# Kernel tuning notes

Hardware: AMD Instinct MI355X
Metric: run time of the kernel (lower is better)

Reference implementation:

```python
import jax, jax.numpy as jnp
import numpy as np

Z = 64
P = Z * Z
H = 4  # hDim_1 = hDim_2 = 2*iDim with iDim=2
EPS = 1e-5
WVAR = 0.1  # WEIGHT_VARIANCE stand-in


def setup_inputs() -> dict:
    key = jax.random.key(0)
    ks = jax.random.split(key, 8)
    B = 4096
    x = jax.random.normal(ks[0], (B, Z), dtype=jnp.float32)
    W1 = jax.random.normal(ks[1], (P, 2, H), dtype=jnp.float32) * WVAR
    b1 = jax.random.normal(ks[2], (P, H), dtype=jnp.float32) * WVAR
    g1 = jnp.ones((P, H), dtype=jnp.float32)
    be1 = jnp.zeros((P, H), dtype=jnp.float32)
    W2 = jax.random.normal(ks[3], (P, H, H), dtype=jnp.float32) * WVAR
    b2 = jax.random.normal(ks[4], (P, H), dtype=jnp.float32) * WVAR
    g2 = jnp.ones((P, H), dtype=jnp.float32)
    be2 = jnp.zeros((P, H), dtype=jnp.float32)
    W3 = jax.random.normal(ks[5], (P, H), dtype=jnp.float32) * WVAR
    b3 = jax.random.normal(ks[6], (P,), dtype=jnp.float32) * WVAR
    return {"x": x, "W1": W1, "b1": b1, "g1": g1, "be1": be1,
            "W2": W2, "b2": b2, "g2": g2, "be2": be2,
            "W3": W3, "b3": b3, "dtPt": B}


def _layernorm(h, g, b):
    # LayerNorm over last dim (size H), biased variance, eps=1e-5 (torch default)
    m = jnp.mean(h, axis=-1, keepdims=True)
    v = jnp.mean(jnp.square(h - m), axis=-1, keepdims=True)
    return (h - m) * jax.lax.rsqrt(v + EPS) * g + b


def reference(x, W1, b1, g1, be1, W2, b2, g2, be2, W3, b3, dtPt):
    B = x.shape[0]
    # pairs[b, z*Z+zp] = (x[b,z], x[b,zp])  -> [B, P, 2]
    a = jnp.broadcast_to(x[:, :, None], (B, Z, Z)).reshape(B, P)
    c = jnp.broadcast_to(x[:, None, :], (B, Z, Z)).reshape(B, P)
    pair = jnp.stack([a, c], axis=-1)  # [B, P, 2]
    h = jnp.einsum('bpi,pih->bph', pair, W1) + b1
    h = _layernorm(jnp.tanh(h), g1, be1)
    h = jnp.einsum('bph,phk->bpk', h, W2) + b2
    h = _layernorm(jnp.tanh(h), g2, be2)
    out = jnp.einsum('bph,ph->bp', h, W3) + b3
    out = jax.nn.sigmoid(out)
    return out.reshape(B, Z, Z)
```

## Files before the change

kernel.cpp:

```cpp
#include <hip/hip_runtime.h>
#include <cstddef>

#define ZDIM 64
#define PDIM 4096
#define PB   256
#define BCHUNK 32

__device__ __forceinline__ float fast_tanh(float x) {
    float e = __builtin_amdgcn_exp2f(x * 2.8853900817779268f);
    float r = __builtin_amdgcn_rcpf(e + 1.0f);
    return __builtin_fmaf(-2.0f, r, 1.0f);
}

__device__ __forceinline__ float fast_sigmoid(float x) {
    float e = __builtin_amdgcn_exp2f(x * -1.4426950408889634f);
    return __builtin_amdgcn_rcpf(e + 1.0f);
}

__global__ void __launch_bounds__(PB) pair_mlp_kernel(
    const float* __restrict__ x,
    const float* __restrict__ W1, const float* __restrict__ b1,
    const float* __restrict__ g1, const float* __restrict__ be1,
    const float* __restrict__ W2, const float* __restrict__ b2,
    const float* __restrict__ g2, const float* __restrict__ be2,
    const float* __restrict__ W3, const float* __restrict__ b3,
    float* __restrict__ out, int nbc)
{
    const int tid = threadIdx.x;
    const int pb  = blockIdx.x / nbc;
    const int bc  = blockIdx.x - pb * nbc;
    const int p   = pb * PB + tid;
    const int z   = __builtin_amdgcn_readfirstlane(p >> 6);
    const int zp  = p & 63;

    const float4* W1v = reinterpret_cast<const float4*>(W1 + (size_t)p * 8);
    const float4 w1x = W1v[0];
    const float4 w1y = W1v[1];
    const float4 b1v  = reinterpret_cast<const float4*>(b1)[p];
    const float4 g1v  = reinterpret_cast<const float4*>(g1)[p];
    const float4 be1v = reinterpret_cast<const float4*>(be1)[p];

    float w2[4][4];
    {
        const float4* W2v = reinterpret_cast<const float4*>(W2 + (size_t)p * 16);
        #pragma unroll
        for (int i = 0; i < 4; ++i) {
            float4 r = W2v[i];
            w2[i][0] = r.x; w2[i][1] = r.y; w2[i][2] = r.z; w2[i][3] = r.w;
        }
    }
    const float4 b2v  = reinterpret_cast<const float4*>(b2)[p];
    const float4 g2v  = reinterpret_cast<const float4*>(g2)[p];
    const float4 be2v = reinterpret_cast<const float4*>(be2)[p];
    const float4 w3v  = reinterpret_cast<const float4*>(W3)[p];
    const float  b3s  = b3[p];

    const float w1aa[4] = {w1x.x, w1x.y, w1x.z, w1x.w};
    const float w1ba[4] = {w1y.x, w1y.y, w1y.z, w1y.w};
    const float b1a[4]  = {b1v.x, b1v.y, b1v.z, b1v.w};
    const float g1a[4]  = {g1v.x, g1v.y, g1v.z, g1v.w};
    const float be1a[4] = {be1v.x, be1v.y, be1v.z, be1v.w};
    const float b2a[4]  = {b2v.x, b2v.y, b2v.z, b2v.w};
    const float g2a[4]  = {g2v.x, g2v.y, g2v.z, g2v.w};
    const float be2a[4] = {be2v.x, be2v.y, be2v.z, be2v.w};
    const float w3a[4]  = {w3v.x, w3v.y, w3v.z, w3v.w};

    float w2g[4][4], cs2[4], b2p[4];
    #pragma unroll
    for (int j = 0; j < 4; ++j) { cs2[j] = 0.f; b2p[j] = b2a[j]; }
    #pragma unroll
    for (int i = 0; i < 4; ++i) {
        #pragma unroll
        for (int j = 0; j < 4; ++j) {
            float wg = g1a[i] * w2[i][j];
            w2g[i][j] = wg;
            cs2[j] += wg;
            b2p[j] = __builtin_fmaf(be1a[i], w2[i][j], b2p[j]);
        }
    }
    float w3g[4], cs3 = 0.f, b3p = b3s;
    #pragma unroll
    for (int j = 0; j < 4; ++j) {
        w3g[j] = g2a[j] * w3a[j];
        cs3 += w3g[j];
        b3p = __builtin_fmaf(be2a[j], w3a[j], b3p);
    }

    const int b0 = bc * BCHUNK;
    for (int it = 0; it < BCHUNK; ++it) {
        const int b = b0 + it;
        const float a = x[b * ZDIM + z];
        const float c = x[b * ZDIM + zp];

        float t[4];
        #pragma unroll
        for (int i = 0; i < 4; ++i)
            t[i] = fast_tanh(__builtin_fmaf(a, w1aa[i],
                         __builtin_fmaf(c, w1ba[i], b1a[i])));

        float s1 = (t[0] + t[1]) + (t[2] + t[3]);
        float s2 = __builtin_fmaf(t[0], t[0],
                   __builtin_fmaf(t[1], t[1],
                   __builtin_fmaf(t[2], t[2], t[3] * t[3])));
        float m  = 0.25f * s1;
        float v  = __builtin_fmaf(0.25f, s2, -(m * m));
        float rs = __builtin_amdgcn_rsqf(v + 1e-5f);

        float u[4];
        #pragma unroll
        for (int j = 0; j < 4; ++j) {
            float acc = -m * cs2[j];
            #pragma unroll
            for (int i = 0; i < 4; ++i)
                acc = __builtin_fmaf(t[i], w2g[i][j], acc);
            u[j] = fast_tanh(__builtin_fmaf(rs, acc, b2p[j]));
        }

        float q1 = (u[0] + u[1]) + (u[2] + u[3]);
        float q2 = __builtin_fmaf(u[0], u[0],
                   __builtin_fmaf(u[1], u[1],
                   __builtin_fmaf(u[2], u[2], u[3] * u[3])));
        float m2  = 0.25f * q1;
        float v2  = __builtin_fmaf(0.25f, q2, -(m2 * m2));
        float rs2 = __builtin_amdgcn_rsqf(v2 + 1e-5f);

        float acc = -m2 * cs3;
        #pragma unroll
        for (int j = 0; j < 4; ++j)
            acc = __builtin_fmaf(u[j], w3g[j], acc);

        out[(size_t)b * PDIM + p] = fast_sigmoid(__builtin_fmaf(rs2, acc, b3p));
    }
}

extern "C" void kernel_launch(void* const* d_in, const int* in_sizes, int n_in,
                              void* d_out, int out_size, void* d_ws, size_t ws_size,
                              hipStream_t stream) {
    const float* x   = (const float*)d_in[0];
    const float* W1  = (const float*)d_in[1];
    const float* b1  = (const float*)d_in[2];
    const float* g1  = (const float*)d_in[3];
    const float* be1 = (const float*)d_in[4];
    const float* W2  = (const float*)d_in[5];
    const float* b2  = (const float*)d_in[6];
    const float* g2  = (const float*)d_in[7];
    const float* be2 = (const float*)d_in[8];
    const float* W3  = (const float*)d_in[9];
    const float* b3  = (const float*)d_in[10];
    float* out = (float*)d_out;

    const int B   = in_sizes[0] / ZDIM;
    const int nbc = B / BCHUNK;
    const int grid = (PDIM / PB) * nbc;

    hipLaunchKernelGGL(pair_mlp_kernel, dim3(grid), dim3(PB), 0, stream,
                       x, W1, b1, g1, be1, W2, b2, g2, be2, W3, b3, out, nbc);
}
```

Measured before the change: 148.5 us.

## Pack batch pairs into v2f FMA and replace exp-based tanh with rational approx

Processes four batch rows per loop iteration, held in two-wide float vectors, so the arithmetic can map onto packed FP32 FMA instructions. Replaces the exp2+rcp tanh with a Padé-style rational polynomial that needs only one reciprocal and otherwise uses packed FMAs, moving work off the transcendental unit. Also adds a minimum-occupancy hint to launch bounds. The rational approximation loses accuracy for large inputs because it does not saturate at ±1, and the wider unroll raises register pressure.

```diff
diff --git a/kernel.cpp b/kernel.cpp
--- a/kernel.cpp
+++ b/kernel.cpp
@@ -6,10 +6,25 @@
 #define PB   256
 #define BCHUNK 32
 
-__device__ __forceinline__ float fast_tanh(float x) {
-    float e = __builtin_amdgcn_exp2f(x * 2.8853900817779268f);
-    float r = __builtin_amdgcn_rcpf(e + 1.0f);
-    return __builtin_fmaf(-2.0f, r, 1.0f);
+typedef float v2f __attribute__((ext_vector_type(2)));
+
+__device__ __forceinline__ v2f pkfma(v2f a, v2f b, v2f c) {
+    return __builtin_elementwise_fma(a, b, c);
+}
+
+__device__ __forceinline__ v2f splat(float s) { v2f r; r.x = s; r.y = s; return r; }
+
+__device__ __forceinline__ v2f tanh2(v2f x) {
+    v2f t = x * x;
+    v2f np = t + splat(378.0f);
+    np = pkfma(np, t, splat(17325.0f));
+    np = pkfma(np, t, splat(135135.0f));
+    v2f dp = pkfma(splat(28.0f), t, splat(3150.0f));
+    dp = pkfma(dp, t, splat(62370.0f));
+    dp = pkfma(dp, t, splat(135135.0f));
+    v2f num = x * np;
+    v2f r; r.x = __builtin_amdgcn_rcpf(dp.x); r.y = __builtin_amdgcn_rcpf(dp.y);
+    return num * r;
 }
 
 __device__ __forceinline__ float fast_sigmoid(float x) {
@@ -17,7 +32,7 @@
     return __builtin_amdgcn_rcpf(e + 1.0f);
 }
 
-__global__ void __launch_bounds__(PB) pair_mlp_kernel(
+__global__ void __launch_bounds__(PB, 4) pair_mlp_kernel(
     const float* __restrict__ x,
     const float* __restrict__ W1, const float* __restrict__ b1,
     const float* __restrict__ g1, const float* __restrict__ be1,
@@ -87,49 +102,82 @@
     }
 
     const int b0 = bc * BCHUNK;
-    for (int it = 0; it < BCHUNK; ++it) {
+    for (int it = 0; it < BCHUNK; it += 4) {
         const int b = b0 + it;
-        const float a = x[b * ZDIM + z];
-        const float c = x[b * ZDIM + zp];
-
-        float t[4];
-        #pragma unroll
-        for (int i = 0; i < 4; ++i)
-            t[i] = fast_tanh(__builtin_fmaf(a, w1aa[i],
-                         __builtin_fmaf(c, w1ba[i], b1a[i])));
-
-        float s1 = (t[0] + t[1]) + (t[2] + t[3]);
-        float s2 = __builtin_fmaf(t[0], t[0],
-                   __builtin_fmaf(t[1], t[1],
-                   __builtin_fmaf(t[2], t[2], t[3] * t[3])));
-        float m  = 0.25f * s1;
-        float v  = __builtin_fmaf(0.25f, s2, -(m * m));
-        float rs = __builtin_amdgcn_rsqf(v + 1e-5f);
-
-        float u[4];
+        v2f avA, cvA, avB, cvB;
+        avA.x = x[(b + 0) * ZDIM + z];
+        avA.y = x[(b + 1) * ZDIM + z];
+        avB.x = x[(b + 2) * ZDIM + z];
+        avB.y = x[(b + 3) * ZDIM + z];
+        cvA.x = x[(b + 0) * ZDIM + zp];
+        cvA.y = x[(b + 1) * ZDIM + zp];
+        cvB.x = x[(b + 2) * ZDIM + zp];
+        cvB.y = x[(b + 3) * ZDIM + zp];
+
+        v2f tA[4], tB[4];
+        #pragma unroll
+        for (int i = 0; i < 4; ++i) {
+            v2f wa = splat(w1aa[i]), wb = splat(w1ba[i]), bb = splat(b1a[i]);
+            tA[i] = tanh2(pkfma(avA, wa, pkfma(cvA, wb, bb)));
+            tB[i] = tanh2(pkfma(avB, wa, pkfma(cvB, wb, bb)));
+        }
+
+        v2f s1A = (tA[0] + tA[1]) + (tA[2] + tA[3]);
+        v2f s1B = (tB[0] + tB[1]) + (tB[2] + tB[3]);
+        v2f s2A = pkfma(tA[0], tA[0], pkfma(tA[1], tA[1], pkfma(tA[2], tA[2], tA[3] * tA[3])));
+        v2f s2B = pkfma(tB[0], tB[0], pkfma(tB[1], tB[1], pkfma(tB[2], tB[2], tB[3] * tB[3])));
+        v2f mA  = s1A * 0.25f,  mB  = s1B * 0.25f;
+        v2f mnA = s1A * -0.25f, mnB = s1B * -0.25f;
+        v2f varA = pkfma(mnA, mA, s2A * 0.25f) + splat(1e-5f);
+        v2f varB = pkfma(mnB, mB, s2B * 0.25f) + splat(1e-5f);
+        v2f rsA, rsB;
+        rsA.x = __builtin_amdgcn_rsqf(varA.x); rsA.y = __builtin_amdgcn_rsqf(varA.y);
+        rsB.x = __builtin_amdgcn_rsqf(varB.x); rsB.y = __builtin_amdgcn_rsqf(varB.y);
+
+        v2f uA[4], uB[4];
         #pragma unroll
         for (int j = 0; j < 4; ++j) {
-            float acc = -m * cs2[j];
+            v2f accA = mnA * splat(cs2[j]);
+            v2f accB = mnB * splat(cs2[j]);
             #pragma unroll
-            for (int i = 0; i < 4; ++i)
-                acc = __builtin_fmaf(t[i], w2g[i][j], acc);
-            u[j] = fast_tanh(__builtin_fmaf(rs, acc, b2p[j]));
-        }
-
-        float q1 = (u[0] + u[1]) + (u[2] + u[3]);
-        float q2 = __builtin_fmaf(u[0], u[0],
-                   __builtin_fmaf(u[1], u[1],
-                   __builtin_fmaf(u[2], u[2], u[3] * u[3])));
-        float m2  = 0.25f * q1;
-        float v2  = __builtin_fmaf(0.25f, q2, -(m2 * m2));
-        float rs2 = __builtin_amdgcn_rsqf(v2 + 1e-5f);
-
-        float acc = -m2 * cs3;
-        #pragma unroll
-        for (int j = 0; j < 4; ++j)
-            acc = __builtin_fmaf(u[j], w3g[j], acc);
-
-        out[(size_t)b * PDIM + p] = fast_sigmoid(__builtin_fmaf(rs2, acc, b3p));
+            for (int i = 0; i < 4; ++i) {
+                v2f wg = splat(w2g[i][j]);
+                accA = pkfma(tA[i], wg, accA);
+                accB = pkfma(tB[i], wg, accB);
+            }
+            v2f bp = splat(b2p[j]);
+            uA[j] = tanh2(pkfma(rsA, accA, bp));
+            uB[j] = tanh2(pkfma(rsB, accB, bp));
+        }
+
+        v2f q1A = (uA[0] + uA[1]) + (uA[2] + uA[3]);
+        v2f q1B = (uB[0] + uB[1]) + (uB[2] + uB[3]);
+        v2f q2A = pkfma(uA[0], uA[0], pkfma(uA[1], uA[1], pkfma(uA[2], uA[2], uA[3] * uA[3])));
+        v2f q2B = pkfma(uB[0], uB[0], pkfma(uB[1], uB[1], pkfma(uB[2], uB[2], uB[3] * uB[3])));
+        v2f m2A  = q1A * 0.25f,  m2B  = q1B * 0.25f;
+        v2f mn2A = q1A * -0.25f, mn2B = q1B * -0.25f;
+        v2f var2A = pkfma(mn2A, m2A, q2A * 0.25f) + splat(1e-5f);
+        v2f var2B = pkfma(mn2B, m2B, q2B * 0.25f) + splat(1e-5f);
+        v2f rs2A, rs2B;
+        rs2A.x = __builtin_amdgcn_rsqf(var2A.x); rs2A.y = __builtin_amdgcn_rsqf(var2A.y);
+        rs2B.x = __builtin_amdgcn_rsqf(var2B.x); rs2B.y = __builtin_amdgcn_rsqf(var2B.y);
+
+        v2f accA = mn2A * splat(cs3);
+        v2f accB = mn2B * splat(cs3);
+        #pragma unroll
+        for (int j = 0; j < 4; ++j) {
+            v2f wg = splat(w3g[j]);
+            accA = pkfma(uA[j], wg, accA);
+            accB = pkfma(uB[j], wg, accB);
+        }
+        v2f bp3 = splat(b3p);
+        v2f sA = pkfma(rs2A, accA, bp3);
+        v2f sB = pkfma(rs2B, accB, bp3);
+
+        out[(size_t)(b + 0) * PDIM + p] = fast_sigmoid(sA.x);
+        out[(size_t)(b + 1) * PDIM + p] = fast_sigmoid(sA.y);
+        out[(size_t)(b + 2) * PDIM + p] = fast_sigmoid(sB.x);
+        out[(size_t)(b + 3) * PDIM + p] = fast_sigmoid(sB.y);
     }
 }
 
```

Measured after the change: 137.5 us. 1.08x faster.

## Vectorize batch pairs with packed FMA and rational tanh approximation

Applied to the files above, without the earlier changes.

Processes two batch rows at once using packed float2 FMA operations, and replaces the exp/rcp tanh with a Padé rational approximation evaluated with packed FMAs and a single reciprocal. Preloads all x values for the chunk into registers, halves the batch chunk to 16, and sets a minimum-occupancy launch bound. The aim is to cut transcendental and scalar ALU issue pressure, at the cost of higher register use and an unclamped tanh approximation that loses accuracy for large arguments.

```diff
diff --git a/kernel.cpp b/kernel.cpp
--- a/kernel.cpp
+++ b/kernel.cpp
@@ -4,20 +4,30 @@
 #define ZDIM 64
 #define PDIM 4096
 #define PB   256
-#define BCHUNK 32
+#define BCHUNK 16
+#define NPAIR (BCHUNK/2)
 
-__device__ __forceinline__ float fast_tanh(float x) {
-    float e = __builtin_amdgcn_exp2f(x * 2.8853900817779268f);
-    float r = __builtin_amdgcn_rcpf(e + 1.0f);
-    return __builtin_fmaf(-2.0f, r, 1.0f);
+typedef float v2f __attribute__((ext_vector_type(2)));
+
+__device__ __forceinline__ v2f pkfma(v2f a, v2f b, v2f c) {
+    return __builtin_elementwise_fma(a, b, c);
+}
+__device__ __forceinline__ v2f splat(float s) { v2f r; r.x = s; r.y = s; return r; }
+
+__device__ __forceinline__ v2f tanh2(v2f x) {
+    v2f t = x * x;
+    v2f np = t + splat(378.0f);
+    np = pkfma(np, t, splat(17325.0f));
+    np = pkfma(np, t, splat(135135.0f));
+    v2f dp = pkfma(splat(28.0f), t, splat(3150.0f));
+    dp = pkfma(dp, t, splat(62370.0f));
+    dp = pkfma(dp, t, splat(135135.0f));
+    v2f num = x * np;
+    v2f r; r.x = __builtin_amdgcn_rcpf(dp.x); r.y = __builtin_amdgcn_rcpf(dp.y);
+    return num * r;
 }
 
-__device__ __forceinline__ float fast_sigmoid(float x) {
-    float e = __builtin_amdgcn_exp2f(x * -1.4426950408889634f);
-    return __builtin_amdgcn_rcpf(e + 1.0f);
-}
-
-__global__ void __launch_bounds__(PB) pair_mlp_kernel(
+__global__ void __launch_bounds__(PB, 3) pair_mlp_kernel(
     const float* __restrict__ x,
     const float* __restrict__ W1, const float* __restrict__ b1,
     const float* __restrict__ g1, const float* __restrict__ be1,
@@ -32,6 +42,15 @@
     const int p   = pb * PB + tid;
     const int z   = __builtin_amdgcn_readfirstlane(p >> 6);
     const int zp  = p & 63;
+    const int b0  = bc * BCHUNK;
+
+    const float* xrow = x + (size_t)b0 * ZDIM;
+    float cvr[BCHUNK], avr[BCHUNK];
+    #pragma unroll
+    for (int r = 0; r < BCHUNK; ++r) {
+        cvr[r] = xrow[r * ZDIM + zp];
+        avr[r] = xrow[r * ZDIM + z];
+    }
 
     const float4* W1v = reinterpret_cast<const float4*>(W1 + (size_t)p * 8);
     const float4 w1x = W1v[0];
@@ -39,7 +58,6 @@
     const float4 b1v  = reinterpret_cast<const float4*>(b1)[p];
     const float4 g1v  = reinterpret_cast<const float4*>(g1)[p];
     const float4 be1v = reinterpret_cast<const float4*>(be1)[p];
-
     float w2[4][4];
     {
         const float4* W2v = reinterpret_cast<const float4*>(W2 + (size_t)p * 16);
@@ -55,81 +73,87 @@
     const float4 w3v  = reinterpret_cast<const float4*>(W3)[p];
     const float  b3s  = b3[p];
 
-    const float w1aa[4] = {w1x.x, w1x.y, w1x.z, w1x.w};
-    const float w1ba[4] = {w1y.x, w1y.y, w1y.z, w1y.w};
-    const float b1a[4]  = {b1v.x, b1v.y, b1v.z, b1v.w};
-    const float g1a[4]  = {g1v.x, g1v.y, g1v.z, g1v.w};
-    const float be1a[4] = {be1v.x, be1v.y, be1v.z, be1v.w};
-    const float b2a[4]  = {b2v.x, b2v.y, b2v.z, b2v.w};
-    const float g2a[4]  = {g2v.x, g2v.y, g2v.z, g2v.w};
-    const float be2a[4] = {be2v.x, be2v.y, be2v.z, be2v.w};
-    const float w3a[4]  = {w3v.x, w3v.y, w3v.z, w3v.w};
+    const float w1a[4] = {w1x.x, w1x.y, w1x.z, w1x.w};
+    const float w1b[4] = {w1y.x, w1y.y, w1y.z, w1y.w};
+    const float b1a[4] = {b1v.x, b1v.y, b1v.z, b1v.w};
+    const float g1a[4] = {g1v.x, g1v.y, g1v.z, g1v.w};
+    const float be1a[4]= {be1v.x, be1v.y, be1v.z, be1v.w};
+    const float b2a[4] = {b2v.x, b2v.y, b2v.z, b2v.w};
+    const float g2a[4] = {g2v.x, g2v.y, g2v.z, g2v.w};
+    const float be2a[4]= {be2v.x, be2v.y, be2v.z, be2v.w};
+    const float w3a[4] = {w3v.x, w3v.y, w3v.z, w3v.w};
 
-    float w2g[4][4], cs2[4], b2p[4];
+    float w2g[4][4], b2p[4];
     #pragma unroll
-    for (int j = 0; j < 4; ++j) { cs2[j] = 0.f; b2p[j] = b2a[j]; }
+    for (int j = 0; j < 4; ++j) b2p[j] = b2a[j];
     #pragma unroll
     for (int i = 0; i < 4; ++i) {
         #pragma unroll
         for (int j = 0; j < 4; ++j) {
-            float wg = g1a[i] * w2[i][j];
-            w2g[i][j] = wg;
-            cs2[j] += wg;
+            w2g[i][j] = g1a[i] * w2[i][j];
             b2p[j] = __builtin_fmaf(be1a[i], w2[i][j], b2p[j]);
         }
     }
-    float w3g[4], cs3 = 0.f, b3p = b3s;
+    float w3g[4], b3p = b3s;
     #pragma unroll
     for (int j = 0; j < 4; ++j) {
         w3g[j] = g2a[j] * w3a[j];
-        cs3 += w3g[j];
         b3p = __builtin_fmaf(be2a[j], w3a[j], b3p);
     }
 
-    const int b0 = bc * BCHUNK;
-    for (int it = 0; it < BCHUNK; ++it) {
-        const int b = b0 + it;
-        const float a = x[b * ZDIM + z];
-        const float c = x[b * ZDIM + zp];
+    float* obase = out + (size_t)b0 * PDIM + p;
 
-        float t[4];
-        #pragma unroll
-        for (int i = 0; i < 4; ++i)
-            t[i] = fast_tanh(__builtin_fmaf(a, w1aa[i],
-                         __builtin_fmaf(c, w1ba[i], b1a[i])));
+    #pragma unroll
+    for (int k = 0; k < NPAIR; ++k) {
+        v2f a2, c2;
+        a2.x = avr[2 * k]; a2.y = avr[2 * k + 1];
+        c2.x = cvr[2 * k]; c2.y = cvr[2 * k + 1];
 
-        float s1 = (t[0] + t[1]) + (t[2] + t[3]);
-        float s2 = __builtin_fmaf(t[0], t[0],
-                   __builtin_fmaf(t[1], t[1],
-                   __builtin_fmaf(t[2], t[2], t[3] * t[3])));
-        float m  = 0.25f * s1;
-        float v  = __builtin_fmaf(0.25f, s2, -(m * m));
-        float rs = __builtin_amdgcn_rsqf(v + 1e-5f);
+        v2f t0 = tanh2(pkfma(a2, splat(w1a[0]), pkfma(c2, splat(w1b[0]), splat(b1a[0]))));
+        v2f t1 = tanh2(pkfma(a2, splat(w1a[1]), pkfma(c2, splat(w1b[1]), splat(b1a[1]))));
+        v2f t2 = tanh2(pkfma(a2, splat(w1a[2]), pkfma(c2, splat(w1b[2]), splat(b1a[2]))));
+        v2f t3 = tanh2(pkfma(a2, splat(w1a[3]), pkfma(c2, splat(w1b[3]), splat(b1a[3]))));
 
-        float u[4];
-        #pragma unroll
-        for (int j = 0; j < 4; ++j) {
-            float acc = -m * cs2[j];
-            #pragma unroll
-            for (int i = 0; i < 4; ++i)
-                acc = __builtin_fmaf(t[i], w2g[i][j], acc);
-            u[j] = fast_tanh(__builtin_fmaf(rs, acc, b2p[j]));
+        v2f s1 = (t0 + t1) + (t2 + t3);
+        v2f s2 = pkfma(t0, t0, pkfma(t1, t1, pkfma(t2, t2, t3 * t3)));
+        v2f m  = s1 * 0.25f;
+        v2f t1e = pkfma(s2, splat(0.25f), splat(1e-5f));
+        v2f var = pkfma(s1 * splat(-0.0625f), s1, t1e);
+        v2f rs; rs.x = __builtin_amdgcn_rsqf(var.x); rs.y = __builtin_amdgcn_rsqf(var.y);
+
+        v2f d0 = t0 - m, d1 = t1 - m, d2 = t2 - m, d3 = t3 - m;
+
+        v2f u0, u1, u2, u3;
+        {
+            v2f acc;
+            acc = pkfma(d0, splat(w2g[0][0]), pkfma(d1, splat(w2g[1][0]), pkfma(d2, splat(w2g[2][0]), d3 * splat(w2g[3][0]))));
+            u0 = tanh2(pkfma(rs, acc, splat(b2p[0])));
+            acc = pkfma(d0, splat(w2g[0][1]), pkfma(d1, splat(w2g[1][1]), pkfma(d2, splat(w2g[2][1]), d3 * splat(w2g[3][1]))));
+            u1 = tanh2(pkfma(rs, acc, splat(b2p[1])));
+            acc = pkfma(d0, splat(w2g[0][2]), pkfma(d1, splat(w2g[1][2]), pkfma(d2, splat(w2g[2][2]), d3 * splat(w2g[3][2]))));
+            u2 = tanh2(pkfma(rs, acc, splat(b2p[2])));
+            acc = pkfma(d0, splat(w2g[0][3]), pkfma(d1, splat(w2g[1][3]), pkfma(d2, splat(w2g[2][3]), d3 * splat(w2g[3][3]))));
+            u3 = tanh2(pkfma(rs, acc, splat(b2p[3])));
         }
 
-        float q1 = (u[0] + u[1]) + (u[2] + u[3]);
-        float q2 = __builtin_fmaf(u[0], u[0],
-                   __builtin_fmaf(u[1], u[1],
-                   __builtin_fmaf(u[2], u[2], u[3] * u[3])));
-        float m2  = 0.25f * q1;
-        float v2  = __builtin_fmaf(0.25f, q2, -(m2 * m2));
-        float rs2 = __builtin_amdgcn_rsqf(v2 + 1e-5f);
+        v2f q1 = (u0 + u1) + (u2 + u3);
+        v2f q2 = pkfma(u0, u0, pkfma(u1, u1, pkfma(u2, u2, u3 * u3)));
+        v2f m2  = q1 * 0.25f;
+        v2f t2e = pkfma(q2, splat(0.25f), splat(1e-5f));
+        v2f var2 = pkfma(q1 * splat(-0.0625f), q1, t2e);
+        v2f rs2; rs2.x = __builtin_amdgcn_rsqf(var2.x); rs2.y = __builtin_amdgcn_rsqf(var2.y);
 
-        float acc = -m2 * cs3;
-        #pragma unroll
-        for (int j = 0; j < 4; ++j)
-            acc = __builtin_fmaf(u[j], w3g[j], acc);
+        v2f e0 = u0 - m2, e1 = u1 - m2, e2 = u2 - m2, e3 = u3 - m2;
 
-        out[(size_t)b * PDIM + p] = fast_sigmoid(__builtin_fmaf(rs2, acc, b3p));
+        v2f acc3 = pkfma(e0, splat(w3g[0]), pkfma(e1, splat(w3g[1]), pkfma(e2, splat(w3g[2]), e3 * splat(w3g[3]))));
+        v2f sarg = pkfma(rs2, acc3, splat(b3p));
+
+        v2f q = sarg * splat(-1.4426950408889634f);
+        v2f e; e.x = __builtin_amdgcn_exp2f(q.x); e.y = __builtin_amdgcn_exp2f(q.y);
+        v2f ep1 = e + splat(1.0f);
+
+        obase[(size_t)(2 * k) * PDIM]     = __builtin_amdgcn_rcpf(ep1.x);
+        obase[(size_t)(2 * k + 1) * PDIM] = __builtin_amdgcn_rcpf(ep1.y);
     }
 }
 
```

New measurement: 137.4 us. 7.5% less time.
